# Performance work log

Hardware: AMD Instinct MI355X
Metric: run time of the kernel (lower is better)

Reference implementation:

```python
import jax, jax.numpy as jnp
import numpy as np

B, N, D, H = 4, 2048, 256, 4
DH = D // H  # 64
TWO_PI = 6.283185307179586


def rotate_half(x):
    # pairs (x0,x1)->(-x1,x0), matching torch unflatten/unbind/stack/flatten
    x1 = x[..., 0::2]
    x2 = x[..., 1::2]
    return jnp.stack((-x2, x1), axis=-1).reshape(x.shape)


def _heads(x):  # [B,N,D] -> [B,H,N,DH]
    return x.reshape(x.shape[0], x.shape[1], H, DH).transpose(0, 2, 1, 3)


def _merge(x):  # [B,H,N,DH] -> [B,N,D]
    return x.transpose(0, 2, 1, 3).reshape(x.shape[0], x.shape[2], H * DH)


def _ffn(x, msg, W1, b1, g, beta, W2, b2):
    h = jnp.concatenate([x, msg], axis=-1) @ W1 + b1
    mu = jnp.mean(h, axis=-1, keepdims=True)
    var = jnp.mean((h - mu) ** 2, axis=-1, keepdims=True)
    h = (h - mu) * jax.lax.rsqrt(var + 1e-5) * g + beta
    h = jax.nn.gelu(h, approximate=False)  # torch nn.GELU() is erf-based
    return x + h @ W2 + b2


def _self_block(d, kp, Wqkv, bqkv, Wo, bo, W1, b1, g, beta, W2, b2):
    b, n = d.shape[0], d.shape[1]
    # torch: unflatten(-1,(H,-1,3)) -> per-head last dim arranged [DH,3]
    qkv = (d @ Wqkv + bqkv).reshape(b, n, H, DH, 3).transpose(0, 2, 1, 3, 4)
    q, k, v = qkv[..., 0], qkv[..., 1], qkv[..., 2]
    q = q * kp[0] + rotate_half(q) * kp[1]
    k = k * kp[0] + rotate_half(k) * kp[1]
    sim = jnp.einsum('bhid,bhjd->bhij', q, k) * (DH ** -0.5)
    a = jax.nn.softmax(sim, axis=-1)
    ctx = _merge(jnp.einsum('bhij,bhjd->bhid', a, v))
    msg = ctx @ Wo + bo
    return _ffn(d, msg, W1, b1, g, beta, W2, b2)


def _sdpa(q, k, v):
    a = jax.nn.softmax(jnp.einsum('bhid,bhjd->bhij', q, k) * (DH ** -0.5), axis=-1)
    return jnp.einsum('bhij,bhjd->bhid', a, v)


def _cross_block(d0, d1, Wqk, bqk, Wv, bv, Wo, bo, W1, b1, g, beta, W2, b2):
    qk0 = _heads(d0 @ Wqk + bqk)
    qk1 = _heads(d1 @ Wqk + bqk)
    v0 = _heads(d0 @ Wv + bv)
    v1 = _heads(d1 @ Wv + bv)
    m0 = _merge(_sdpa(qk0, qk1, v1)) @ Wo + bo
    m1 = _merge(_sdpa(qk1, qk0, v0)) @ Wo + bo
    return _ffn(d0, m0, W1, b1, g, beta, W2, b2), _ffn(d1, m1, W1, b1, g, beta, W2, b2)


def setup_inputs() -> dict:
    key = jax.random.key(0)
    ks = jax.random.split(key, 32)
    def w(k, shape, fan_in):
        return jax.random.normal(k, shape, jnp.float32) / np.sqrt(fan_in)
    ang0 = jax.random.uniform(ks[0], (B, 1, N, DH), jnp.float32) * TWO_PI
    ang1 = jax.random.uniform(ks[1], (B, 1, N, DH), jnp.float32) * TWO_PI
    inp = {
        'keypoints0': jnp.stack([jnp.cos(ang0), jnp.sin(ang0)]),
        'keypoints1': jnp.stack([jnp.cos(ang1), jnp.sin(ang1)]),
        'descriptors0': jax.random.normal(ks[2], (B, N, D), jnp.float32),
        'descriptors1': jax.random.normal(ks[3], (B, N, D), jnp.float32),
        'sa_Wqkv': w(ks[4], (D, 3 * D), D), 'sa_bqkv': w(ks[5], (3 * D,), D),
        'sa_Wo': w(ks[6], (D, D), D), 'sa_bo': w(ks[7], (D,), D),
        'sa_W1': w(ks[8], (2 * D, 2 * D), 2 * D), 'sa_b1': w(ks[9], (2 * D,), 2 * D),
        'sa_g': jnp.ones((2 * D,), jnp.float32), 'sa_beta': jnp.zeros((2 * D,), jnp.float32),
        'sa_W2': w(ks[10], (2 * D, D), 2 * D), 'sa_b2': w(ks[11], (D,), 2 * D),
        'ca_Wqk': w(ks[12], (D, D), D), 'ca_bqk': w(ks[13], (D,), D),
        'ca_Wv': w(ks[14], (D, D), D), 'ca_bv': w(ks[15], (D,), D),
        'ca_Wo': w(ks[16], (D, D), D), 'ca_bo': w(ks[17], (D,), D),
        'ca_W1': w(ks[18], (2 * D, 2 * D), 2 * D), 'ca_b1': w(ks[19], (2 * D,), 2 * D),
        'ca_g': jnp.ones((2 * D,), jnp.float32), 'ca_beta': jnp.zeros((2 * D,), jnp.float32),
        'ca_W2': w(ks[20], (2 * D, D), 2 * D), 'ca_b2': w(ks[21], (D,), 2 * D),
    }
    return inp


def reference(keypoints0, keypoints1, descriptors0, descriptors1,
              sa_Wqkv, sa_bqkv, sa_Wo, sa_bo, sa_W1, sa_b1, sa_g, sa_beta, sa_W2, sa_b2,
              ca_Wqk, ca_bqk, ca_Wv, ca_bv, ca_Wo, ca_bo, ca_W1, ca_b1, ca_g, ca_beta, ca_W2, ca_b2):
    d0 = _self_block(descriptors0, keypoints0, sa_Wqkv, sa_bqkv, sa_Wo, sa_bo,
                     sa_W1, sa_b1, sa_g, sa_beta, sa_W2, sa_b2)
    d1 = _self_block(descriptors1, keypoints1, sa_Wqkv, sa_bqkv, sa_Wo, sa_bo,
                     sa_W1, sa_b1, sa_g, sa_beta, sa_W2, sa_b2)
    return _cross_block(d0, d1, ca_Wqk, ca_bqk, ca_Wv, ca_bv, ca_Wo, ca_bo,
                        ca_W1, ca_b1, ca_g, ca_beta, ca_W2, ca_b2)
```

## Files before the change

kernel.cpp:

```cpp
#include <hip/hip_runtime.h>
#include <hip/hip_bf16.h>

typedef unsigned short u16;
typedef short bf16x8 __attribute__((ext_vector_type(8)));
typedef unsigned short u16x8 __attribute__((ext_vector_type(8)));
typedef float f32x4 __attribute__((ext_vector_type(4)));
typedef float f32x16 __attribute__((ext_vector_type(16)));

#define NB 4
#define NS 2048
#define DM 256
#define NH 4
#define DHD 64
#define MR (NB*NS)
#define BHC (NB*NH)
#define ACH 8
#define ACK (NS/ACH)

__device__ __forceinline__ u16 f2b(float f){
    __hip_bfloat16 h = __float2bfloat16(f);
    return __builtin_bit_cast(u16, h);
}
__device__ __forceinline__ float b2f(u16 u){
    unsigned v = ((unsigned)u) << 16; float f; __builtin_memcpy(&f, &v, 4); return f;
}
__device__ __forceinline__ float fexp2(float x){
    float r; asm("v_exp_f32 %0, %1" : "=v"(r) : "v"(x)); return r;
}

#define MFMA16(a,b,c) __builtin_amdgcn_mfma_f32_16x16x32_bf16((a),(b),(c),0,0,0)
#define MFMA32(a,b,c) __builtin_amdgcn_mfma_f32_32x32x16_bf16((a),(b),(c),0,0,0)

__global__ void k_cast_bf16(const float* __restrict__ src, u16* __restrict__ dst, int n){
    int i = (blockIdx.x*blockDim.x + threadIdx.x)*4;
    if (i + 3 < n){
        float4 v = *(const float4*)(src + i);
        dst[i+0] = f2b(v.x); dst[i+1] = f2b(v.y); dst[i+2] = f2b(v.z); dst[i+3] = f2b(v.w);
    }
}
__global__ void k_cast_w_t(const float* __restrict__ W, u16* __restrict__ Wt, int K, int Nc){
    int idx = blockIdx.x*blockDim.x + threadIdx.x;
    if (idx >= K*Nc) return;
    int k = idx % K, nc = idx / K;
    Wt[idx] = f2b(W[(size_t)k*Nc + nc]);
}
__global__ void k_fill_x(const u16* __restrict__ Xb, u16* __restrict__ cat){
    int i = blockIdx.x*256 + threadIdx.x;
    if (i >= MR*DM/8) return;
    int row = i >> 5, c8 = i & 31;
    *(u16x8*)(cat + (size_t)row*512 + c8*8) = *(const u16x8*)(Xb + (size_t)row*256 + c8*8);
}

#define GEMM_CORE(Aptr, Wptr, Kdim) \
    __shared__ __attribute__((aligned(16))) u16 As[64*72]; \
    __shared__ __attribute__((aligned(16))) u16 Bs[64*72]; \
    const int tid = threadIdx.x; \
    const int lane = tid & 63, widx = tid >> 6; \
    const int wr = widx >> 1, wc = widx & 1; \
    const int r16 = lane & 15, g = lane >> 4; \
    const int m0 = blockIdx.x * 64, n0 = blockIdx.y * 64; \
    f32x4 acc[2][2] = {}; \
    { const int nkt = (Kdim) >> 6; \
    for (int kt = 0; kt < nkt; ++kt){ \
        _Pragma("unroll") \
        for (int it = 0; it < 2; ++it){ \
            int ch = tid + it*256; \
            int row = ch >> 3, cc = ch & 7; \
            *(u16x8*)(As + row*72 + cc*8) = *(const u16x8*)((Aptr) + (size_t)(m0+row)*(Kdim) + kt*64 + cc*8); \
            *(u16x8*)(Bs + row*72 + cc*8) = *(const u16x8*)((Wptr) + (size_t)(n0+row)*(Kdim) + kt*64 + cc*8); \
        } \
        __syncthreads(); \
        _Pragma("unroll") \
        for (int s = 0; s < 2; ++s){ \
            bf16x8 a0 = *(const bf16x8*)(As + (wr*32 +      r16)*72 + s*32 + g*8); \
            bf16x8 a1 = *(const bf16x8*)(As + (wr*32 + 16 + r16)*72 + s*32 + g*8); \
            bf16x8 b0 = *(const bf16x8*)(Bs + (wc*32 +      r16)*72 + s*32 + g*8); \
            bf16x8 b1 = *(const bf16x8*)(Bs + (wc*32 + 16 + r16)*72 + s*32 + g*8); \
            acc[0][0] = MFMA16(a0, b0, acc[0][0]); \
            acc[0][1] = MFMA16(a0, b1, acc[0][1]); \
            acc[1][0] = MFMA16(a1, b0, acc[1][0]); \
            acc[1][1] = MFMA16(a1, b1, acc[1][1]); \
        } \
        __syncthreads(); \
    } }

__global__ __launch_bounds__(256) void k_gemm(const u16* __restrict__ A, const u16* __restrict__ Wt,
                                              const float* __restrict__ bias, float* __restrict__ C,
                                              int K, int Nc){
    GEMM_CORE(A, Wt, K)
#pragma unroll
    for (int mi = 0; mi < 2; ++mi)
#pragma unroll
    for (int ni = 0; ni < 2; ++ni){
        int row = m0 + wr*32 + mi*16 + g*4;
        int col = n0 + wc*32 + ni*16 + r16;
        float bc = bias[col];
        float* cp = C + (size_t)row*Nc + col;
#pragma unroll
        for (int rr = 0; rr < 4; ++rr) cp[(size_t)rr*Nc] = acc[mi][ni][rr] + bc;
    }
}
__global__ __launch_bounds__(256) void k_gemm_cat(const u16* __restrict__ A, const u16* __restrict__ Wt,
                                                  const float* __restrict__ bias, u16* __restrict__ cat,
                                                  int K){
    GEMM_CORE(A, Wt, K)
#pragma unroll
    for (int mi = 0; mi < 2; ++mi)
#pragma unroll
    for (int ni = 0; ni < 2; ++ni){
        int row = m0 + wr*32 + mi*16 + g*4;
        int col = n0 + wc*32 + ni*16 + r16;
        float bc = bias[col];
        u16* cp = cat + (size_t)row*512 + 256 + col;
#pragma unroll
        for (int rr = 0; rr < 4; ++rr) cp[(size_t)rr*512] = f2b(acc[mi][ni][rr] + bc);
    }
}
__global__ __launch_bounds__(256) void k_gemm_qk(const u16* __restrict__ A, const u16* __restrict__ Wt,
                                                 const float* __restrict__ bias, u16* __restrict__ Q,
                                                 int K){
    GEMM_CORE(A, Wt, K)
#pragma unroll
    for (int mi = 0; mi < 2; ++mi)
#pragma unroll
    for (int ni = 0; ni < 2; ++ni){
        int row = m0 + wr*32 + mi*16 + g*4;
        int col = n0 + wc*32 + ni*16 + r16;
        float bc = bias[col];
        int h = col >> 6, dh = col & 63;
#pragma unroll
        for (int rr = 0; rr < 4; ++rr){
            int r2 = row + rr;
            int b = r2 >> 11, n = r2 & (NS-1);
            Q[((size_t)(b*NH + h)*NS + n)*DHD + dh] = f2b(acc[mi][ni][rr] + bc);
        }
    }
}
template<bool WRITEB>
__global__ __launch_bounds__(256) void k_gemm_resid(const u16* __restrict__ A, const u16* __restrict__ Wt,
                                                    const float* __restrict__ bias, const float* __restrict__ X,
                                                    float* __restrict__ OutF, u16* __restrict__ OutB,
                                                    int K, int Nc){
    GEMM_CORE(A, Wt, K)
#pragma unroll
    for (int mi = 0; mi < 2; ++mi)
#pragma unroll
    for (int ni = 0; ni < 2; ++ni){
        int row = m0 + wr*32 + mi*16 + g*4;
        int col = n0 + wc*32 + ni*16 + r16;
        float bc = bias[col];
#pragma unroll
        for (int rr = 0; rr < 4; ++rr){
            size_t idx = (size_t)(row+rr)*Nc + col;
            float v = acc[mi][ni][rr] + bc + X[idx];
            OutF[idx] = v;
            if (WRITEB) OutB[idx] = f2b(v);
        }
    }
}

__global__ void k_qkv_epi(const float* __restrict__ C, const float* __restrict__ kp,
                          u16* __restrict__ Q, u16* __restrict__ K, u16* __restrict__ VT){
    int idx = blockIdx.x*blockDim.x + threadIdx.x;
    if (idx >= BHC*NS*32) return;
    int dhp = idx & 31;
    int n   = (idx >> 5) & (NS-1);
    int bh  = idx >> 16;
    int b = bh >> 2, h = bh & 3;
    size_t crow = (size_t)(b*NS + n)*768 + h*192 + dhp*6;
    float q0 = C[crow+0], k0 = C[crow+1], v0 = C[crow+2];
    float q1 = C[crow+3], k1 = C[crow+4], v1 = C[crow+5];
    size_t kb = (size_t)b*(NS*DHD) + (size_t)n*DHD + dhp*2;
    float c0 = kp[kb], c1 = kp[kb+1];
    float s0 = kp[kb + (size_t)NB*NS*DHD], s1 = kp[kb + (size_t)NB*NS*DHD + 1];
    float qr0 = q0*c0 - q1*s0, qr1 = q1*c1 + q0*s1;
    float kr0 = k0*c0 - k1*s0, kr1 = k1*c1 + k0*s1;
    size_t qk = ((size_t)bh*NS + n)*DHD + dhp*2;
    Q[qk]   = f2b(qr0); Q[qk+1] = f2b(qr1);
    K[qk]   = f2b(kr0); K[qk+1] = f2b(kr1);
    size_t vt = ((size_t)bh*DHD + dhp*2)*NS + n;
    VT[vt]      = f2b(v0);
    VT[vt + NS] = f2b(v1);
}
__global__ void k_v_epi(const float* __restrict__ C, u16* __restrict__ VT){
    int idx = blockIdx.x*blockDim.x + threadIdx.x;
    if (idx >= BHC*NS*DHD) return;
    int n = idx & (NS-1); int dh = (idx >> 11) & 63; int bh = idx >> 17;
    int b = bh >> 2, h = bh & 3;
    VT[idx] = f2b(C[(size_t)(b*NS + n)*DM + h*DHD + dh]);
}

__global__ __launch_bounds__(256) void k_attn3(const u16* __restrict__ Q, const u16* __restrict__ Kb,
                                               const u16* __restrict__ VT,
                                               u16* __restrict__ opart, float* __restrict__ mpart,
                                               float* __restrict__ lpart, float scale_l2e){
    const int tid = threadIdx.x, lane = tid & 63, widx = tid >> 6;
    const int l31 = lane & 31, hi = lane >> 5;
    const int gw = blockIdx.x*4 + widx;
    const int bh = gw >> 6, qt = gw & 63;
    const int q0 = qt * 32;
    const int ck = blockIdx.y;

    bf16x8 qf[4];
    {
        const u16* Qp = Q + ((size_t)bh*NS + q0 + l31)*DHD + hi*8;
#pragma unroll
        for (int kk = 0; kk < 4; ++kk){
            u16x8 raw = *(const u16x8*)(Qp + kk*16);
            u16x8 sc;
#pragma unroll
            for (int i = 0; i < 8; ++i) sc[i] = f2b(b2f(raw[i]) * scale_l2e);
            qf[kk] = __builtin_bit_cast(bf16x8, sc);
        }
    }

    f32x16 o0 = {}, o1 = {};
    float m_run = -1e30f, l_run = 0.f;
    const u16* Kbase = Kb + ((size_t)bh*NS + ck*ACK)*DHD;
    const u16* Vb0 = VT + ((size_t)bh*DHD +      l31)*NS + ck*ACK;
    const u16* Vb1 = VT + ((size_t)bh*DHD + 32 + l31)*NS + ck*ACK;

    for (int jt = 0; jt < ACK/32; ++jt){
        const u16* Kp = Kbase + (size_t)(jt*32 + l31)*DHD + hi*8;
        f32x16 s = {};
#pragma unroll
        for (int kk = 0; kk < 4; ++kk){
            bf16x8 kf = *(const bf16x8*)(Kp + kk*16);
            s = MFMA32(kf, qf[kk], s);
        }
        float t[8];
#pragma unroll
        for (int i = 0; i < 8; ++i) t[i] = fmaxf(s[2*i], s[2*i+1]);
#pragma unroll
        for (int i = 0; i < 4; ++i) t[i] = fmaxf(t[i], t[i+4]);
        t[0] = fmaxf(t[0], t[2]); t[1] = fmaxf(t[1], t[3]);
        float mx = fmaxf(t[0], t[1]);
        mx = fmaxf(mx, __shfl_xor(mx, 32));
        if (__any(mx > m_run + 8.0f)){
            float mn = fmaxf(m_run, mx);
            float corr = fexp2(m_run - mn);
            l_run *= corr;
            o0 *= corr; o1 *= corr;
            m_run = mn;
        }
        float p[16];
#pragma unroll
        for (int i = 0; i < 16; ++i) p[i] = fexp2(s[i] - m_run);
        float u[8];
#pragma unroll
        for (int i = 0; i < 8; ++i) u[i] = p[2*i] + p[2*i+1];
#pragma unroll
        for (int i = 0; i < 4; ++i) u[i] = u[i] + u[i+4];
        u[0] += u[2]; u[1] += u[3];
        float sum = u[0] + u[1];
        sum += __shfl_xor(sum, 32);
        l_run += sum;
        unsigned c[8], x[8];
#pragma unroll
        for (int i = 0; i < 8; ++i)
            c[i] = ((unsigned)f2b(p[2*i+1]) << 16) | (unsigned)f2b(p[2*i]);
#pragma unroll
        for (int i = 0; i < 8; ++i) x[i] = __shfl_xor(c[i], 32);
        unsigned pb0w[4], pb1w[4];
        pb0w[0] = hi ? x[2] : c[0];  pb0w[1] = hi ? x[3] : c[1];
        pb0w[2] = hi ? c[2] : x[0];  pb0w[3] = hi ? c[3] : x[1];
        pb1w[0] = hi ? x[6] : c[4];  pb1w[1] = hi ? x[7] : c[5];
        pb1w[2] = hi ? c[6] : x[4];  pb1w[3] = hi ? c[7] : x[5];
        bf16x8 pb0, pb1;
        __builtin_memcpy(&pb0, pb0w, 16);
        __builtin_memcpy(&pb1, pb1w, 16);
        bf16x8 v00 = *(const bf16x8*)(Vb0 + jt*32 +      hi*8);
        bf16x8 v01 = *(const bf16x8*)(Vb0 + jt*32 + 16 + hi*8);
        bf16x8 v10 = *(const bf16x8*)(Vb1 + jt*32 +      hi*8);
        bf16x8 v11 = *(const bf16x8*)(Vb1 + jt*32 + 16 + hi*8);
        o0 = MFMA32(v00, pb0, o0);
        o0 = MFMA32(v01, pb1, o0);
        o1 = MFMA32(v10, pb0, o1);
        o1 = MFMA32(v11, pb1, o1);
    }
    const size_t rq = ((size_t)ck*BHC + bh)*NS + q0 + l31;
    if (!hi){ mpart[rq] = m_run; lpart[rq] = l_run; }
    u16* op = opart + rq*64;
#pragma unroll
    for (int r = 0; r < 16; ++r){
        int d = (r & 3) + 8*(r >> 2) + 4*hi;
        op[d]      = f2b(o0[r]);
        op[d + 32] = f2b(o1[r]);
    }
}

__global__ __launch_bounds__(256) void k_attn_comb(const u16* __restrict__ opart,
                                                   const float* __restrict__ mpart,
                                                   const float* __restrict__ lpart,
                                                   u16* __restrict__ ctx){
    int idx = blockIdx.x*256 + threadIdx.x;
    if (idx >= BHC*NS*64) return;
    int d = idx & 63; int n = (idx >> 6) & (NS-1); int bh = idx >> 17;
    size_t row = (size_t)bh*NS + n;
    const size_t CH = (size_t)BHC*NS;
    float M = -1e30f;
#pragma unroll
    for (int ck = 0; ck < ACH; ++ck) M = fmaxf(M, mpart[ck*CH + row]);
    float l = 0.f, o = 0.f;
#pragma unroll
    for (int ck = 0; ck < ACH; ++ck){
        float e = fexp2(mpart[ck*CH + row] - M);
        l += lpart[ck*CH + row] * e;
        o += b2f(opart[(ck*CH + row)*64 + d]) * e;
    }
    int b = bh >> 2, h = bh & 3;
    ctx[((size_t)b*NS + n)*DM + h*DHD + d] = f2b(o / l);
}

__global__ __launch_bounds__(256) void k_ln_gelu(const float* __restrict__ C, const float* __restrict__ gam,
                                                 const float* __restrict__ bet, u16* __restrict__ hb){
    int row = blockIdx.x, t = threadIdx.x;
    const float* cr = C + (size_t)row*512;
    float x0 = cr[t], x1 = cr[t+256];
    float s = x0 + x1, q = x0*x0 + x1*x1;
#pragma unroll
    for (int offs = 1; offs < 64; offs <<= 1){
        s += __shfl_xor(s, offs);
        q += __shfl_xor(q, offs);
    }
    __shared__ float ss[4], qq[4];
    int w = t >> 6, ln = t & 63;
    if (ln == 0){ ss[w] = s; qq[w] = q; }
    __syncthreads();
    s = ss[0]+ss[1]+ss[2]+ss[3];
    q = qq[0]+qq[1]+qq[2]+qq[3];
    float mu = s * (1.f/512.f);
    float var = q * (1.f/512.f) - mu*mu;
    float rs = rsqrtf(var + 1e-5f);
    float y0 = (x0 - mu)*rs*gam[t]     + bet[t];
    float y1 = (x1 - mu)*rs*gam[t+256] + bet[t+256];
    float g0 = 0.5f*y0*(1.f + erff(y0*0.70710678118654752f));
    float g1 = 0.5f*y1*(1.f + erff(y1*0.70710678118654752f));
    hb[(size_t)row*512 + t]       = f2b(g0);
    hb[(size_t)row*512 + 256 + t] = f2b(g1);
}

extern "C" void kernel_launch(void* const* d_in, const int* in_sizes, int n_in,
                              void* d_out, int out_size, void* d_ws, size_t ws_size,
                              hipStream_t stream)
{
    const float* kp0   = (const float*)d_in[0];
    const float* kp1   = (const float*)d_in[1];
    const float* desc0 = (const float*)d_in[2];
    const float* desc1 = (const float*)d_in[3];
    const float* saWqkv= (const float*)d_in[4];
    const float* sabqkv= (const float*)d_in[5];
    const float* saWo  = (const float*)d_in[6];
    const float* sabo  = (const float*)d_in[7];
    const float* saW1  = (const float*)d_in[8];
    const float* sab1  = (const float*)d_in[9];
    const float* sag   = (const float*)d_in[10];
    const float* sabe  = (const float*)d_in[11];
    const float* saW2  = (const float*)d_in[12];
    const float* sab2  = (const float*)d_in[13];
    const float* caWqk = (const float*)d_in[14];
    const float* cabqk = (const float*)d_in[15];
    const float* caWv  = (const float*)d_in[16];
    const float* cabv  = (const float*)d_in[17];
    const float* caWo  = (const float*)d_in[18];
    const float* cabo  = (const float*)d_in[19];
    const float* caW1  = (const float*)d_in[20];
    const float* cab1  = (const float*)d_in[21];
    const float* cag   = (const float*)d_in[22];
    const float* cabe  = (const float*)d_in[23];
    const float* caW2  = (const float*)d_in[24];
    const float* cab2  = (const float*)d_in[25];

    char* ws = (char*)d_ws;
    size_t off = 0;
    auto alloc = [&](size_t b)->char*{ char* p = ws + off; off = (off + b + 255) & ~(size_t)255; return p; };

    u16* wqkvT = (u16*)alloc(768*256*2);
    u16* woST  = (u16*)alloc(256*256*2);
    u16* w1ST  = (u16*)alloc(512*512*2);
    u16* w2ST  = (u16*)alloc(256*512*2);
    u16* wqkT  = (u16*)alloc(256*256*2);
    u16* wvT   = (u16*)alloc(256*256*2);
    u16* woCT  = (u16*)alloc(256*256*2);
    u16* w1CT  = (u16*)alloc(512*512*2);
    u16* w2CT  = (u16*)alloc(256*512*2);
    u16* X0b   = (u16*)alloc((size_t)MR*DM*2);
    u16* X1b   = (u16*)alloc((size_t)MR*DM*2);
    u16* Qb    = (u16*)alloc((size_t)MR*DM*2);
    u16* Kbf   = (u16*)alloc((size_t)MR*DM*2);
    u16* VTa   = (u16*)alloc((size_t)MR*DM*2);
    u16* VT0   = (u16*)alloc((size_t)MR*DM*2);
    u16* ctxb  = (u16*)alloc((size_t)MR*DM*2);
    u16* midb0 = (u16*)alloc((size_t)MR*DM*2);
    u16* midb1 = (u16*)alloc((size_t)MR*DM*2);
    u16* catb  = (u16*)alloc((size_t)MR*512*2);
    u16* hb    = (u16*)alloc((size_t)MR*512*2);
    char* uni  = alloc((size_t)ACH*BHC*NS*64*2);
    float* Cbuf = (float*)uni;
    u16*  opart = (u16*)uni;
    float* mid0= (float*)alloc((size_t)MR*DM*4);
    float* mid1= (float*)alloc((size_t)MR*DM*4);
    float* mpart = (float*)alloc((size_t)ACH*BHC*NS*4);
    float* lpart = (float*)alloc((size_t)ACH*BHC*NS*4);

    k_cast_w_t<<<768, 256, 0, stream>>>(saWqkv, wqkvT, 256, 768);
    k_cast_w_t<<<256, 256, 0, stream>>>(saWo,  woST, 256, 256);
    k_cast_w_t<<<1024,256, 0, stream>>>(saW1,  w1ST, 512, 512);
    k_cast_w_t<<<512, 256, 0, stream>>>(saW2,  w2ST, 512, 256);
    k_cast_w_t<<<256, 256, 0, stream>>>(caWqk, wqkT, 256, 256);
    k_cast_w_t<<<256, 256, 0, stream>>>(caWv,  wvT,  256, 256);
    k_cast_w_t<<<256, 256, 0, stream>>>(caWo,  woCT, 256, 256);
    k_cast_w_t<<<1024,256, 0, stream>>>(caW1,  w1CT, 512, 512);
    k_cast_w_t<<<512, 256, 0, stream>>>(caW2,  w2CT, 512, 256);
    k_cast_bf16<<<2048, 256, 0, stream>>>(desc0, X0b, MR*DM);
    k_cast_bf16<<<2048, 256, 0, stream>>>(desc1, X1b, MR*DM);

    const dim3 AG(256, ACH);
    const float SC = 0.125f * 1.44269504088896f;

    k_gemm<<<dim3(128,12),256,0,stream>>>(X0b, wqkvT, sabqkv, Cbuf, 256, 768);
    k_qkv_epi<<<4096,256,0,stream>>>(Cbuf, kp0, Qb, Kbf, VTa);
    k_attn3<<<AG,256,0,stream>>>(Qb, Kbf, VTa, opart, mpart, lpart, SC);
    k_attn_comb<<<8192,256,0,stream>>>(opart, mpart, lpart, ctxb);
    k_fill_x<<<1024,256,0,stream>>>(X0b, catb);
    k_gemm_cat<<<dim3(128,4),256,0,stream>>>(ctxb, woST, sabo, catb, 256);
    k_gemm<<<dim3(128,8),256,0,stream>>>(catb, w1ST, sab1, Cbuf, 512, 512);
    k_ln_gelu<<<8192,256,0,stream>>>(Cbuf, sag, sabe, hb);
    k_gemm_resid<true><<<dim3(128,4),256,0,stream>>>(hb, w2ST, sab2, desc0, mid0, midb0, 512, 256);

    k_gemm<<<dim3(128,12),256,0,stream>>>(X1b, wqkvT, sabqkv, Cbuf, 256, 768);
    k_qkv_epi<<<4096,256,0,stream>>>(Cbuf, kp1, Qb, Kbf, VTa);
    k_attn3<<<AG,256,0,stream>>>(Qb, Kbf, VTa, opart, mpart, lpart, SC);
    k_attn_comb<<<8192,256,0,stream>>>(opart, mpart, lpart, ctxb);
    k_fill_x<<<1024,256,0,stream>>>(X1b, catb);
    k_gemm_cat<<<dim3(128,4),256,0,stream>>>(ctxb, woST, sabo, catb, 256);
    k_gemm<<<dim3(128,8),256,0,stream>>>(catb, w1ST, sab1, Cbuf, 512, 512);
    k_ln_gelu<<<8192,256,0,stream>>>(Cbuf, sag, sabe, hb);
    k_gemm_resid<true><<<dim3(128,4),256,0,stream>>>(hb, w2ST, sab2, desc1, mid1, midb1, 512, 256);

    k_gemm_qk<<<dim3(128,4),256,0,stream>>>(midb0, wqkT, cabqk, Qb, 256);
    k_gemm_qk<<<dim3(128,4),256,0,stream>>>(midb1, wqkT, cabqk, Kbf, 256);
    k_gemm<<<dim3(128,4),256,0,stream>>>(midb1, wvT, cabv, Cbuf, 256, 256);
    k_v_epi<<<8192,256,0,stream>>>(Cbuf, VTa);
    k_gemm<<<dim3(128,4),256,0,stream>>>(midb0, wvT, cabv, Cbuf, 256, 256);
    k_v_epi<<<8192,256,0,stream>>>(Cbuf, VT0);

    float* out0 = (float*)d_out;
    float* out1 = out0 + (size_t)MR*DM;

    k_attn3<<<AG,256,0,stream>>>(Qb, Kbf, VTa, opart, mpart, lpart, SC);
    k_attn_comb<<<8192,256,0,stream>>>(opart, mpart, lpart, ctxb);
    k_fill_x<<<1024,256,0,stream>>>(midb0, catb);
    k_gemm_cat<<<dim3(128,4),256,0,stream>>>(ctxb, woCT, cabo, catb, 256);
    k_gemm<<<dim3(128,8),256,0,stream>>>(catb, w1CT, cab1, Cbuf, 512, 512);
    k_ln_gelu<<<8192,256,0,stream>>>(Cbuf, cag, cabe, hb);
    k_gemm_resid<false><<<dim3(128,4),256,0,stream>>>(hb, w2CT, cab2, mid0, out0, nullptr, 512, 256);

    k_attn3<<<AG,256,0,stream>>>(Kbf, Qb, VT0, opart, mpart, lpart, SC);
    k_attn_comb<<<8192,256,0,stream>>>(opart, mpart, lpart, ctxb);
    k_fill_x<<<1024,256,0,stream>>>(midb1, catb);
    k_gemm_cat<<<dim3(128,4),256,0,stream>>>(ctxb, woCT, cabo, catb, 256);
    k_gemm<<<dim3(128,8),256,0,stream>>>(catb, w1CT, cab1, Cbuf, 512, 512);
    k_ln_gelu<<<8192,256,0,stream>>>(Cbuf, cag, cabe, hb);
    k_gemm_resid<false><<<dim3(128,4),256,0,stream>>>(hb, w2CT, cab2, mid1, out1, nullptr, 512, 256);

    (void)in_sizes; (void)n_in; (void)out_size; (void)ws_size;
}
```

Measured before the change: 621.8 us.

## Batch both descriptor streams into single launches for attention, FFN and casts

Both images are processed together. Self-attention and cross-attention run as one attention launch over 32 batch-head slices, and the Wo, FFN, LayerNorm-GELU and residual GEMMs run over twice as many rows. The key-split factor drops from 8 to 4 because the grid is now larger. The nine weight casts and two descriptor casts become five combined kernels. The V epilogue is fused into a transposing GEMM store, the Q/K projection writes both destinations at once, and the final residual now reads bf16 mid activations instead of fp32. The aim is to remove launch overhead and under-filled grids, at the cost of a slightly less precise residual and larger shared workspaces.

```diff
diff --git a/kernel.cpp b/kernel.cpp
--- a/kernel.cpp
+++ b/kernel.cpp
@@ -14,8 +14,11 @@
 #define DHD 64
 #define MR (NB*NS)
 #define BHC (NB*NH)
-#define ACH 8
+#define BH2 32
+#define M2 (2*MR)
+#define ACH 4
 #define ACK (NS/ACH)
+#define HS ((size_t)BHC*NS*DHD)
 
 __device__ __forceinline__ u16 f2b(float f){
     __hip_bfloat16 h = __float2bfloat16(f);
@@ -31,22 +34,43 @@
 #define MFMA16(a,b,c) __builtin_amdgcn_mfma_f32_16x16x32_bf16((a),(b),(c),0,0,0)
 #define MFMA32(a,b,c) __builtin_amdgcn_mfma_f32_32x32x16_bf16((a),(b),(c),0,0,0)
 
-__global__ void k_cast_bf16(const float* __restrict__ src, u16* __restrict__ dst, int n){
-    int i = (blockIdx.x*blockDim.x + threadIdx.x)*4;
-    if (i + 3 < n){
-        float4 v = *(const float4*)(src + i);
-        dst[i+0] = f2b(v.x); dst[i+1] = f2b(v.y); dst[i+2] = f2b(v.z); dst[i+3] = f2b(v.w);
-    }
-}
-__global__ void k_cast_w_t(const float* __restrict__ W, u16* __restrict__ Wt, int K, int Nc){
-    int idx = blockIdx.x*blockDim.x + threadIdx.x;
-    if (idx >= K*Nc) return;
+__global__ void k_cast_desc(const float* __restrict__ d0, const float* __restrict__ d1, u16* __restrict__ dst){
+    int i = (blockIdx.x*256 + threadIdx.x)*4;
+    if (i + 3 >= 2*MR*DM) return;
+    const float* src = (i < MR*DM) ? d0 : d1;
+    int j = (i < MR*DM) ? i : i - MR*DM;
+    float4 v = *(const float4*)(src + j);
+    dst[i+0] = f2b(v.x); dst[i+1] = f2b(v.y); dst[i+2] = f2b(v.z); dst[i+3] = f2b(v.w);
+}
+__device__ __forceinline__ void wt_one(const float* W, u16* Wt, int idx, int K, int Nc){
     int k = idx % K, nc = idx / K;
     Wt[idx] = f2b(W[(size_t)k*Nc + nc]);
 }
+__global__ void k_cwt1(const float* __restrict__ W, u16* __restrict__ Wt, int K, int Nc){
+    int idx = blockIdx.x*256 + threadIdx.x;
+    if (idx < K*Nc) wt_one(W, Wt, idx, K, Nc);
+}
+__global__ void k_cwt4(const float* W0, const float* W1, const float* W2, const float* W3,
+                       u16* T0, u16* T1, u16* T2, u16* T3){
+    int idx = blockIdx.x*256 + threadIdx.x;
+    int w = idx >> 16, j = idx & 65535;
+    const float* W = (w==0)?W0:(w==1)?W1:(w==2)?W2:W3;
+    u16* T = (w==0)?T0:(w==1)?T1:(w==2)?T2:T3;
+    wt_one(W, T, j, 256, 256);
+}
+__global__ void k_cwt2a(const float* W0, const float* W1, u16* T0, u16* T1){
+    int idx = blockIdx.x*256 + threadIdx.x;
+    int w = idx >> 18, j = idx & 262143;
+    wt_one(w? W1:W0, w? T1:T0, j, 512, 512);
+}
+__global__ void k_cwt2b(const float* W0, const float* W1, u16* T0, u16* T1){
+    int idx = blockIdx.x*256 + threadIdx.x;
+    int w = idx >> 17, j = idx & 131071;
+    wt_one(w? W1:W0, w? T1:T0, j, 512, 256);
+}
 __global__ void k_fill_x(const u16* __restrict__ Xb, u16* __restrict__ cat){
     int i = blockIdx.x*256 + threadIdx.x;
-    if (i >= MR*DM/8) return;
+    if (i >= M2*DM/8) return;
     int row = i >> 5, c8 = i & 31;
     *(u16x8*)(cat + (size_t)row*512 + c8*8) = *(const u16x8*)(Xb + (size_t)row*256 + c8*8);
 }
@@ -117,8 +141,8 @@
     }
 }
 __global__ __launch_bounds__(256) void k_gemm_qk(const u16* __restrict__ A, const u16* __restrict__ Wt,
-                                                 const float* __restrict__ bias, u16* __restrict__ Q,
-                                                 int K){
+                                                 const float* __restrict__ bias,
+                                                 u16* __restrict__ dstQ, u16* __restrict__ dstK, int K){
     GEMM_CORE(A, Wt, K)
 #pragma unroll
     for (int mi = 0; mi < 2; ++mi)
@@ -132,29 +156,68 @@
         for (int rr = 0; rr < 4; ++rr){
             int r2 = row + rr;
             int b = r2 >> 11, n = r2 & (NS-1);
-            Q[((size_t)(b*NH + h)*NS + n)*DHD + dh] = f2b(acc[mi][ni][rr] + bc);
-        }
-    }
-}
-template<bool WRITEB>
-__global__ __launch_bounds__(256) void k_gemm_resid(const u16* __restrict__ A, const u16* __restrict__ Wt,
-                                                    const float* __restrict__ bias, const float* __restrict__ X,
-                                                    float* __restrict__ OutF, u16* __restrict__ OutB,
-                                                    int K, int Nc){
-    GEMM_CORE(A, Wt, K)
-#pragma unroll
-    for (int mi = 0; mi < 2; ++mi)
-#pragma unroll
-    for (int ni = 0; ni < 2; ++ni){
-        int row = m0 + wr*32 + mi*16 + g*4;
-        int col = n0 + wc*32 + ni*16 + r16;
-        float bc = bias[col];
+            u16 v = f2b(acc[mi][ni][rr] + bc);
+            size_t off = ((size_t)(b*NH + h)*NS + n)*DHD + dh;
+            dstQ[off] = v;
+            dstK[off] = v;
+        }
+    }
+}
+__global__ __launch_bounds__(256) void k_gemm_vt(const u16* __restrict__ A, const u16* __restrict__ Wt,
+                                                 const float* __restrict__ bias, u16* __restrict__ VT, int K){
+    GEMM_CORE(A, Wt, K)
+#pragma unroll
+    for (int mi = 0; mi < 2; ++mi)
+#pragma unroll
+    for (int ni = 0; ni < 2; ++ni){
+        int row = m0 + wr*32 + mi*16 + g*4;
+        int col = n0 + wc*32 + ni*16 + r16;
+        float bc = bias[col];
+        int h = col >> 6, dh = col & 63;
 #pragma unroll
         for (int rr = 0; rr < 4; ++rr){
-            size_t idx = (size_t)(row+rr)*Nc + col;
-            float v = acc[mi][ni][rr] + bc + X[idx];
-            OutF[idx] = v;
-            if (WRITEB) OutB[idx] = f2b(v);
+            int r2 = row + rr;
+            int b = r2 >> 11, n = r2 & (NS-1);
+            VT[((size_t)(b*NH + h)*DHD + dh)*NS + n] = f2b(acc[mi][ni][rr] + bc);
+        }
+    }
+}
+__global__ __launch_bounds__(256) void k_gemm_resid_mid(const u16* __restrict__ A, const u16* __restrict__ Wt,
+                                                        const float* __restrict__ bias,
+                                                        const float* __restrict__ X0, const float* __restrict__ X1,
+                                                        u16* __restrict__ OutB, int K){
+    GEMM_CORE(A, Wt, K)
+#pragma unroll
+    for (int mi = 0; mi < 2; ++mi)
+#pragma unroll
+    for (int ni = 0; ni < 2; ++ni){
+        int row = m0 + wr*32 + mi*16 + g*4;
+        int col = n0 + wc*32 + ni*16 + r16;
+        float bc = bias[col];
+#pragma unroll
+        for (int rr = 0; rr < 4; ++rr){
+            int r2 = row + rr;
+            const float* X = (r2 < MR) ? X0 : X1;
+            size_t xi = (size_t)(r2 < MR ? r2 : r2 - MR)*DM + col;
+            OutB[(size_t)r2*DM + col] = f2b(acc[mi][ni][rr] + bc + X[xi]);
+        }
+    }
+}
+__global__ __launch_bounds__(256) void k_gemm_resid_out(const u16* __restrict__ A, const u16* __restrict__ Wt,
+                                                        const float* __restrict__ bias,
+                                                        const u16* __restrict__ Xb, float* __restrict__ OutF, int K){
+    GEMM_CORE(A, Wt, K)
+#pragma unroll
+    for (int mi = 0; mi < 2; ++mi)
+#pragma unroll
+    for (int ni = 0; ni < 2; ++ni){
+        int row = m0 + wr*32 + mi*16 + g*4;
+        int col = n0 + wc*32 + ni*16 + r16;
+        float bc = bias[col];
+#pragma unroll
+        for (int rr = 0; rr < 4; ++rr){
+            size_t idx = (size_t)(row+rr)*DM + col;
+            OutF[idx] = acc[mi][ni][rr] + bc + b2f(Xb[idx]);
         }
     }
 }
@@ -182,13 +245,6 @@
     VT[vt]      = f2b(v0);
     VT[vt + NS] = f2b(v1);
 }
-__global__ void k_v_epi(const float* __restrict__ C, u16* __restrict__ VT){
-    int idx = blockIdx.x*blockDim.x + threadIdx.x;
-    if (idx >= BHC*NS*DHD) return;
-    int n = idx & (NS-1); int dh = (idx >> 11) & 63; int bh = idx >> 17;
-    int b = bh >> 2, h = bh & 3;
-    VT[idx] = f2b(C[(size_t)(b*NS + n)*DM + h*DHD + dh]);
-}
 
 __global__ __launch_bounds__(256) void k_attn3(const u16* __restrict__ Q, const u16* __restrict__ Kb,
                                                const u16* __restrict__ VT,
@@ -278,7 +334,7 @@
         o1 = MFMA32(v10, pb0, o1);
         o1 = MFMA32(v11, pb1, o1);
     }
-    const size_t rq = ((size_t)ck*BHC + bh)*NS + q0 + l31;
+    const size_t rq = ((size_t)ck*BH2 + bh)*NS + q0 + l31;
     if (!hi){ mpart[rq] = m_run; lpart[rq] = l_run; }
     u16* op = opart + rq*64;
 #pragma unroll
@@ -294,10 +350,10 @@
                                                    const float* __restrict__ lpart,
                                                    u16* __restrict__ ctx){
     int idx = blockIdx.x*256 + threadIdx.x;
-    if (idx >= BHC*NS*64) return;
-    int d = idx & 63; int n = (idx >> 6) & (NS-1); int bh = idx >> 17;
-    size_t row = (size_t)bh*NS + n;
-    const size_t CH = (size_t)BHC*NS;
+    if (idx >= BH2*NS*64) return;
+    int d = idx & 63; int n = (idx >> 6) & (NS-1); int bh2 = idx >> 17;
+    size_t row = (size_t)bh2*NS + n;
+    const size_t CH = (size_t)BH2*NS;
     float M = -1e30f;
 #pragma unroll
     for (int ck = 0; ck < ACH; ++ck) M = fmaxf(M, mpart[ck*CH + row]);
@@ -308,8 +364,9 @@
         l += lpart[ck*CH + row] * e;
         o += b2f(opart[(ck*CH + row)*64 + d]) * e;
     }
+    int side = bh2 >> 4, bh = bh2 & 15;
     int b = bh >> 2, h = bh & 3;
-    ctx[((size_t)b*NS + n)*DM + h*DHD + d] = f2b(o / l);
+    ctx[((size_t)side*MR + (size_t)b*NS + n)*DM + h*DHD + d] = f2b(o / l);
 }
 
 __global__ __launch_bounds__(256) void k_ln_gelu(const float* __restrict__ C, const float* __restrict__ gam,
@@ -384,85 +441,53 @@
     u16* woCT  = (u16*)alloc(256*256*2);
     u16* w1CT  = (u16*)alloc(512*512*2);
     u16* w2CT  = (u16*)alloc(256*512*2);
-    u16* X0b   = (u16*)alloc((size_t)MR*DM*2);
-    u16* X1b   = (u16*)alloc((size_t)MR*DM*2);
-    u16* Qb    = (u16*)alloc((size_t)MR*DM*2);
-    u16* Kbf   = (u16*)alloc((size_t)MR*DM*2);
-    u16* VTa   = (u16*)alloc((size_t)MR*DM*2);
-    u16* VT0   = (u16*)alloc((size_t)MR*DM*2);
-    u16* ctxb  = (u16*)alloc((size_t)MR*DM*2);
-    u16* midb0 = (u16*)alloc((size_t)MR*DM*2);
-    u16* midb1 = (u16*)alloc((size_t)MR*DM*2);
-    u16* catb  = (u16*)alloc((size_t)MR*512*2);
-    u16* hb    = (u16*)alloc((size_t)MR*512*2);
-    char* uni  = alloc((size_t)ACH*BHC*NS*64*2);
+    u16* X01b  = (u16*)alloc((size_t)M2*DM*2);
+    u16* Q2    = (u16*)alloc((size_t)BH2*NS*DHD*2);
+    u16* K2    = (u16*)alloc((size_t)BH2*NS*DHD*2);
+    u16* V2    = (u16*)alloc((size_t)BH2*NS*DHD*2);
+    u16* ctx2  = (u16*)alloc((size_t)M2*DM*2);
+    u16* midb2 = (u16*)alloc((size_t)M2*DM*2);
+    u16* cat2  = (u16*)alloc((size_t)M2*512*2);
+    u16* hb2   = cat2;
+    char* uni  = alloc(33554432);
     float* Cbuf = (float*)uni;
     u16*  opart = (u16*)uni;
-    float* mid0= (float*)alloc((size_t)MR*DM*4);
-    float* mid1= (float*)alloc((size_t)MR*DM*4);
-    float* mpart = (float*)alloc((size_t)ACH*BHC*NS*4);
-    float* lpart = (float*)alloc((size_t)ACH*BHC*NS*4);
-
-    k_cast_w_t<<<768, 256, 0, stream>>>(saWqkv, wqkvT, 256, 768);
-    k_cast_w_t<<<256, 256, 0, stream>>>(saWo,  woST, 256, 256);
-    k_cast_w_t<<<1024,256, 0, stream>>>(saW1,  w1ST, 512, 512);
-    k_cast_w_t<<<512, 256, 0, stream>>>(saW2,  w2ST, 512, 256);
-    k_cast_w_t<<<256, 256, 0, stream>>>(caWqk, wqkT, 256, 256);
-    k_cast_w_t<<<256, 256, 0, stream>>>(caWv,  wvT,  256, 256);
-    k_cast_w_t<<<256, 256, 0, stream>>>(caWo,  woCT, 256, 256);
-    k_cast_w_t<<<1024,256, 0, stream>>>(caW1,  w1CT, 512, 512);
-    k_cast_w_t<<<512, 256, 0, stream>>>(caW2,  w2CT, 512, 256);
-    k_cast_bf16<<<2048, 256, 0, stream>>>(desc0, X0b, MR*DM);
-    k_cast_bf16<<<2048, 256, 0, stream>>>(desc1, X1b, MR*DM);
-
-    const dim3 AG(256, ACH);
+    float* mpart = (float*)alloc((size_t)ACH*BH2*NS*4);
+    float* lpart = (float*)alloc((size_t)ACH*BH2*NS*4);
+
+    k_cwt1 <<<768, 256, 0, stream>>>(saWqkv, wqkvT, 256, 768);
+    k_cwt4 <<<1024,256, 0, stream>>>(saWo, caWqk, caWv, caWo, woST, wqkT, wvT, woCT);
+    k_cwt2a<<<2048,256, 0, stream>>>(saW1, caW1, w1ST, w1CT);
+    k_cwt2b<<<1024,256, 0, stream>>>(saW2, caW2, w2ST, w2CT);
+    k_cast_desc<<<4096,256,0,stream>>>(desc0, desc1, X01b);
+
+    const dim3 AG(512, ACH);
     const float SC = 0.125f * 1.44269504088896f;
 
-    k_gemm<<<dim3(128,12),256,0,stream>>>(X0b, wqkvT, sabqkv, Cbuf, 256, 768);
-    k_qkv_epi<<<4096,256,0,stream>>>(Cbuf, kp0, Qb, Kbf, VTa);
-    k_attn3<<<AG,256,0,stream>>>(Qb, Kbf, VTa, opart, mpart, lpart, SC);
-    k_attn_comb<<<8192,256,0,stream>>>(opart, mpart, lpart, ctxb);
-    k_fill_x<<<1024,256,0,stream>>>(X0b, catb);
-    k_gemm_cat<<<dim3(128,4),256,0,stream>>>(ctxb, woST, sabo, catb, 256);
-    k_gemm<<<dim3(128,8),256,0,stream>>>(catb, w1ST, sab1, Cbuf, 512, 512);
-    k_ln_gelu<<<8192,256,0,stream>>>(Cbuf, sag, sabe, hb);
-    k_gemm_resid<true><<<dim3(128,4),256,0,stream>>>(hb, w2ST, sab2, desc0, mid0, midb0, 512, 256);
-
-    k_gemm<<<dim3(128,12),256,0,stream>>>(X1b, wqkvT, sabqkv, Cbuf, 256, 768);
-    k_qkv_epi<<<4096,256,0,stream>>>(Cbuf, kp1, Qb, Kbf, VTa);
-    k_attn3<<<AG,256,0,stream>>>(Qb, Kbf, VTa, opart, mpart, lpart, SC);
-    k_attn_comb<<<8192,256,0,stream>>>(opart, mpart, lpart, ctxb);
-    k_fill_x<<<1024,256,0,stream>>>(X1b, catb);
-    k_gemm_cat<<<dim3(128,4),256,0,stream>>>(ctxb, woST, sabo, catb, 256);
-    k_gemm<<<dim3(128,8),256,0,stream>>>(catb, w1ST, sab1, Cbuf, 512, 512);
-    k_ln_gelu<<<8192,256,0,stream>>>(Cbuf, sag, sabe, hb);
-    k_gemm_resid<true><<<dim3(128,4),256,0,stream>>>(hb, w2ST, sab2, desc1, mid1, midb1, 512, 256);
-
-    k_gemm_qk<<<dim3(128,4),256,0,stream>>>(midb0, wqkT, cabqk, Qb, 256);
-    k_gemm_qk<<<dim3(128,4),256,0,stream>>>(midb1, wqkT, cabqk, Kbf, 256);
-    k_gemm<<<dim3(128,4),256,0,stream>>>(midb1, wvT, cabv, Cbuf, 256, 256);
-    k_v_epi<<<8192,256,0,stream>>>(Cbuf, VTa);
-    k_gemm<<<dim3(128,4),256,0,stream>>>(midb0, wvT, cabv, Cbuf, 256, 256);
-    k_v_epi<<<8192,256,0,stream>>>(Cbuf, VT0);
-
-    float* out0 = (float*)d_out;
-    float* out1 = out0 + (size_t)MR*DM;
-
-    k_attn3<<<AG,256,0,stream>>>(Qb, Kbf, VTa, opart, mpart, lpart, SC);
-    k_attn_comb<<<8192,256,0,stream>>>(opart, mpart, lpart, ctxb);
-    k_fill_x<<<1024,256,0,stream>>>(midb0, catb);
-    k_gemm_cat<<<dim3(128,4),256,0,stream>>>(ctxb, woCT, cabo, catb, 256);
-    k_gemm<<<dim3(128,8),256,0,stream>>>(catb, w1CT, cab1, Cbuf, 512, 512);
-    k_ln_gelu<<<8192,256,0,stream>>>(Cbuf, cag, cabe, hb);
-    k_gemm_resid<false><<<dim3(128,4),256,0,stream>>>(hb, w2CT, cab2, mid0, out0, nullptr, 512, 256);
-
-    k_attn3<<<AG,256,0,stream>>>(Kbf, Qb, VT0, opart, mpart, lpart, SC);
-    k_attn_comb<<<8192,256,0,stream>>>(opart, mpart, lpart, ctxb);
-    k_fill_x<<<1024,256,0,stream>>>(midb1, catb);
-    k_gemm_cat<<<dim3(128,4),256,0,stream>>>(ctxb, woCT, cabo, catb, 256);
-    k_gemm<<<dim3(128,8),256,0,stream>>>(catb, w1CT, cab1, Cbuf, 512, 512);
-    k_ln_gelu<<<8192,256,0,stream>>>(Cbuf, cag, cabe, hb);
-    k_gemm_resid<false><<<dim3(128,4),256,0,stream>>>(hb, w2CT, cab2, mid1, out1, nullptr, 512, 256);
+    k_gemm<<<dim3(128,12),256,0,stream>>>(X01b,            wqkvT, sabqkv, Cbuf, 256, 768);
+    k_qkv_epi<<<4096,256,0,stream>>>(Cbuf, kp0, Q2, K2, V2);
+    k_gemm<<<dim3(128,12),256,0,stream>>>(X01b + (size_t)MR*DM, wqkvT, sabqkv, Cbuf, 256, 768);
+    k_qkv_epi<<<4096,256,0,stream>>>(Cbuf, kp1, Q2 + HS, K2 + HS, V2 + HS);
+    k_attn3<<<AG,256,0,stream>>>(Q2, K2, V2, opart, mpart, lpart, SC);
+    k_attn_comb<<<16384,256,0,stream>>>(opart, mpart, lpart, ctx2);
+    k_fill_x<<<2048,256,0,stream>>>(X01b, cat2);
+    k_gemm_cat<<<dim3(256,4),256,0,stream>>>(ctx2, woST, sabo, cat2, 256);
+    k_gemm<<<dim3(256,8),256,0,stream>>>(cat2, w1ST, sab1, Cbuf, 512, 512);
+    k_ln_gelu<<<16384,256,0,stream>>>(Cbuf, sag, sabe, hb2);
+    k_gemm_resid_mid<<<dim3(256,4),256,0,stream>>>(hb2, w2ST, sab2, desc0, desc1, midb2, 512);
+
+    k_gemm_qk<<<dim3(128,4),256,0,stream>>>(midb2,                wqkT, cabqk, Q2,      K2 + HS, 256);
+    k_gemm_qk<<<dim3(128,4),256,0,stream>>>(midb2 + (size_t)MR*DM, wqkT, cabqk, Q2 + HS, K2,      256);
+    k_gemm_vt<<<dim3(128,4),256,0,stream>>>(midb2 + (size_t)MR*DM, wvT,  cabv,  V2,      256);
+    k_gemm_vt<<<dim3(128,4),256,0,stream>>>(midb2,                wvT,  cabv,  V2 + HS, 256);
+
+    k_attn3<<<AG,256,0,stream>>>(Q2, K2, V2, opart, mpart, lpart, SC);
+    k_attn_comb<<<16384,256,0,stream>>>(opart, mpart, lpart, ctx2);
+    k_fill_x<<<2048,256,0,stream>>>(midb2, cat2);
+    k_gemm_cat<<<dim3(256,4),256,0,stream>>>(ctx2, woCT, cabo, cat2, 256);
+    k_gemm<<<dim3(256,8),256,0,stream>>>(cat2, w1CT, cab1, Cbuf, 512, 512);
+    k_ln_gelu<<<16384,256,0,stream>>>(Cbuf, cag, cabe, hb2);
+    k_gemm_resid_out<<<dim3(256,4),256,0,stream>>>(hb2, w2CT, cab2, midb2, (float*)d_out, 512);
 
     (void)in_sizes; (void)n_in; (void)out_size; (void)ws_size;
 }
```

Result: faster. 505.4 us (-18.7%).
